# Kernel tuning notes

Measured on AMD Instinct MI355X. Metric: run time of the kernel, lower is better.

## Reference

```python
import jax, jax.numpy as jnp
import numpy as np


def setup_inputs() -> dict:
    key = jax.random.key(0)
    ks = jax.random.split(key, 5)
    N, D, H, E = 4096, 1024, 4096, 8
    x = jax.random.normal(ks[0], (N, D), dtype=jnp.float32)
    gate_w = jax.random.normal(ks[1], (D, E), dtype=jnp.float32) * (1.0 / np.sqrt(D))
    gate_b = jnp.zeros((E,), dtype=jnp.float32)
    W1 = jax.random.normal(ks[2], (E, D, H), dtype=jnp.float32) * (1.0 / np.sqrt(D))
    b1 = jnp.zeros((E, H), dtype=jnp.float32)
    W2 = jax.random.normal(ks[3], (E, H, D), dtype=jnp.float32) * (1.0 / np.sqrt(H))
    b2 = jnp.zeros((E, D), dtype=jnp.float32)
    return {"x": x, "gate_w": gate_w, "gate_b": gate_b,
            "W1": W1, "b1": b1, "W2": W2, "b2": b2}


def reference(x, gate_w, gate_b, W1, b1, W2, b2):
    # x: [N, D]; W1: [E, D, H]; W2: [E, H, D]
    K = 2
    N, D = x.shape
    E = gate_w.shape[1]
    logits = x @ gate_w + gate_b                      # [N, E]
    probs = jax.nn.softmax(logits, axis=-1)           # [N, E]
    topw, topi = jax.lax.top_k(probs, K)              # [N, K] each; raw probs, not renormalized
    # combine weights as dense [N, E] (zero for unselected experts)
    combine = jnp.zeros((N, E), dtype=x.dtype).at[jnp.arange(N)[:, None], topi].add(topw)
    # batched expert MLP over all experts (dense-dispatch; math identical to top-k combine)
    h = jnp.einsum('nd,edh->enh', x, W1) + b1[:, None, :]   # [E, N, H]
    h = jax.nn.gelu(h, approximate=True)                     # tanh-approx GELU
    y = jnp.einsum('enh,ehd->end', h, W2) + b2[:, None, :]   # [E, N, D]
    out = jnp.einsum('end,ne->nd', y, combine)               # weighted combine
    return out
```

## Files before the change

### kernel.cpp

```cpp
#include <hip/hip_runtime.h>
#include <cstdint>
#include <cstddef>

#define DEVI __device__ __forceinline__

constexpr int N_TOK = 4096, DIM = 1024, HID = 4096, NE = 8;
constexpr int NKR = N_TOK * 2;

typedef __attribute__((ext_vector_type(8))) short short8;
typedef __attribute__((ext_vector_type(4))) float f32x4;

DEVI ushort f2bf(float f) {
  union { float f; uint32_t u; } v; v.f = f;
  uint32_t r = v.u + 0x7FFFu + ((v.u >> 16) & 1u);
  return (ushort)(r >> 16);
}

DEVI float gelu_t(float x) {
  float t = 0.7978845608028654f * (x + 0.044715f * x * x * x);
  t = fminf(fmaxf(t, -15.f), 15.f);
  float e = __expf(2.f * t);
  return 0.5f * x * (1.f + (e - 1.f) / (e + 1.f));
}

DEVI void gload_lds16(const ushort* g, ushort* l) {
  __builtin_amdgcn_global_load_lds(
      (const __attribute__((address_space(1))) void*)g,
      (__attribute__((address_space(3))) void*)l, 16, 0, 0);
}

__global__ void zero_out_kernel(float* __restrict__ out, int n) {
  int i = blockIdx.x * 256 + threadIdx.x;
  if (i < n) out[i] = 0.f;
}

__global__ void convert_x_kernel(const float* __restrict__ x, ushort* __restrict__ xbf) {
  int i = (blockIdx.x * 256 + threadIdx.x) * 4;
  float4 v = *(const float4*)(x + i);
  ushort4 o;
  o.x = f2bf(v.x); o.y = f2bf(v.y); o.z = f2bf(v.z); o.w = f2bf(v.w);
  *(ushort4*)(xbf + i) = o;
}

template<int R, int C>
__global__ void transpose_bf16(const float* __restrict__ src, ushort* __restrict__ dst) {
  __shared__ ushort t[64][68];
  int e = blockIdx.z;
  const float* s = src + (size_t)e * R * C;
  ushort* d = dst + (size_t)e * R * C;
  int r0 = blockIdx.y * 64, c0 = blockIdx.x * 64;
  int lr = threadIdx.x >> 4;
  int lc = (threadIdx.x & 15) * 4;
#pragma unroll
  for (int i = 0; i < 4; ++i) {
    int r = lr + i * 16;
    float4 v = *(const float4*)(s + (size_t)(r0 + r) * C + c0 + lc);
    t[lc + 0][r] = f2bf(v.x);
    t[lc + 1][r] = f2bf(v.y);
    t[lc + 2][r] = f2bf(v.z);
    t[lc + 3][r] = f2bf(v.w);
  }
  __syncthreads();
#pragma unroll
  for (int i = 0; i < 4; ++i) {
    int c = lr + i * 16;
    ushort4 o = *(const ushort4*)&t[c][lc];
    *(ushort4*)(d + (size_t)(c0 + c) * R + r0 + lc) = o;
  }
}

__global__ void gate_kernel(const float* __restrict__ x, const float* __restrict__ gw,
                            const float* __restrict__ gb,
                            int* __restrict__ topi, float* __restrict__ topw,
                            int* __restrict__ counts) {
  int n = blockIdx.x;
  int lane = threadIdx.x;
  double p[NE];
#pragma unroll
  for (int e = 0; e < NE; ++e) p[e] = 0.0;
  const float* xr = x + (size_t)n * DIM;
  for (int d = lane; d < DIM; d += 64) {
    float xv = xr[d];
    const float* g = gw + (size_t)d * NE;
#pragma unroll
    for (int e = 0; e < NE; ++e) p[e] += (double)xv * (double)g[e];
  }
#pragma unroll
  for (int e = 0; e < NE; ++e) {
#pragma unroll
    for (int s = 32; s > 0; s >>= 1) p[e] += __shfl_down(p[e], s);
  }
  if (lane == 0) {
    double m = -1e300;
#pragma unroll
    for (int e = 0; e < NE; ++e) { p[e] += (double)gb[e]; if (p[e] > m) m = p[e]; }
    double s = 0.0, ex[NE];
#pragma unroll
    for (int e = 0; e < NE; ++e) { ex[e] = exp(p[e] - m); s += ex[e]; }
    double inv = 1.0 / s;
    int e0 = 0, e1 = 0; double v0 = -1.0, v1 = -1.0;
#pragma unroll
    for (int e = 0; e < NE; ++e) {
      double pe = ex[e] * inv;
      if (pe > v0)      { v1 = v0; e1 = e0; v0 = pe; e0 = e; }
      else if (pe > v1) { v1 = pe; e1 = e; }
    }
    topi[n * 2] = e0; topi[n * 2 + 1] = e1;
    topw[n * 2] = (float)v0; topw[n * 2 + 1] = (float)v1;
    atomicAdd(&counts[e0], 1);
    atomicAdd(&counts[e1], 1);
  }
}

__global__ void prefix_kernel(const int* __restrict__ counts, int* __restrict__ offs) {
  if (threadIdx.x == 0) {
    int s = 0;
    for (int e = 0; e < NE; ++e) { offs[e] = s; s += counts[e]; }
  }
}

__global__ void scatter_kernel(const int* __restrict__ topi, const float* __restrict__ topw,
                               const int* __restrict__ offs, int* __restrict__ fill,
                               int* __restrict__ tok, float* __restrict__ wgt) {
  int n = blockIdx.x * blockDim.x + threadIdx.x;
  if (n >= N_TOK) return;
#pragma unroll
  for (int k = 0; k < 2; ++k) {
    int e = topi[n * 2 + k];
    int pos = atomicAdd(&fill[e], 1);
    int g = offs[e] + pos;
    tok[g] = n;
    wgt[g] = topw[n * 2 + k];
  }
}

template<int K, int NX, bool FIRST>
__global__ __launch_bounds__(256) void moe_gemm(
    const ushort* __restrict__ A,
    const ushort* __restrict__ B,
    const float* __restrict__ bias,
    const int* __restrict__ tok, const float* __restrict__ wgt,
    const int* __restrict__ offs, const int* __restrict__ counts,
    ushort* __restrict__ hbuf, float* __restrict__ out)
{
  constexpr int NCOL = FIRST ? HID : DIM;
  constexpr int TSZ = 128 * 64;
  __shared__ ushort Asm[2 * TSZ];
  __shared__ ushort Bsm[2 * TSZ];

  const int nwg = NX * 32 * NE;
  const int bid = blockIdx.x;
  const int swz = (bid & 7) * (nwg >> 3) + (bid >> 3);
  const int e = swz / (NX * 32);
  const int rem = swz - e * (NX * 32);
  const int xt = rem >> 5;
  const int yt = rem & 31;

  const int cnt = counts[e];
  const int mbase = yt * 128;
  if (mbase >= cnt) return;
  const int off = offs[e];
  const int nbase = xt * 128;
  int rv = cnt - mbase; if (rv > 128) rv = 128;

  const int tid = threadIdx.x;
  const int lane = tid & 63, wave = tid >> 6;
  const int sr = tid >> 3;
  const int sc = (tid & 7) * 8;

  const ushort* arow[4];
  const ushort* brow[4];
  const ushort* Be = B + (size_t)e * ((size_t)HID * DIM) + (size_t)nbase * K;
#pragma unroll
  for (int i = 0; i < 4; ++i) {
    int r = sr + 32 * i;
    int rc = r < rv ? r : rv - 1;
    int g = off + mbase + rc;
    long t = FIRST ? (long)tok[g] : (long)g;
    arow[i] = A + t * (long)K + sc;
    brow[i] = Be + (size_t)r * K + sc;
  }

  f32x4 acc[4][4];
#pragma unroll
  for (int a = 0; a < 4; ++a)
#pragma unroll
    for (int b = 0; b < 4; ++b) acc[a][b] = (f32x4)0.f;

  const int quad = lane >> 4, lrow = lane & 15;
  const int wm = (wave >> 1) * 64, wn = (wave & 1) * 64;

  auto stage = [&](int buf, int k0) {
#pragma unroll
    for (int i = 0; i < 4; ++i) {
      gload_lds16(arow[i] + k0, &Asm[buf * TSZ + (i * 32 + wave * 8) * 64]);
      gload_lds16(brow[i] + k0, &Bsm[buf * TSZ + (i * 32 + wave * 8) * 64]);
    }
  };
  auto compute = [&](int buf) {
#pragma unroll
    for (int ks = 0; ks < 2; ++ks) {
      short8 af[4], bf[4];
#pragma unroll
      for (int mt = 0; mt < 4; ++mt)
        af[mt] = *(const short8*)&Asm[buf * TSZ + (wm + mt * 16 + lrow) * 64 + ks * 32 + quad * 8];
#pragma unroll
      for (int nt = 0; nt < 4; ++nt)
        bf[nt] = *(const short8*)&Bsm[buf * TSZ + (wn + nt * 16 + lrow) * 64 + ks * 32 + quad * 8];
#pragma unroll
      for (int mt = 0; mt < 4; ++mt)
#pragma unroll
        for (int nt = 0; nt < 4; ++nt)
          acc[mt][nt] = __builtin_amdgcn_mfma_f32_16x16x32_bf16(af[mt], bf[nt], acc[mt][nt], 0, 0, 0);
    }
  };

  constexpr int NK = K / 64;
  stage(0, 0);
  int cur = 0;
  for (int t = 0; t + 1 < NK; ++t) {
    stage(cur ^ 1, (t + 1) * 64);
    asm volatile("s_waitcnt vmcnt(8)" ::: "memory");
    __builtin_amdgcn_s_barrier();
    __builtin_amdgcn_sched_barrier(0);
    compute(cur);
    __builtin_amdgcn_sched_barrier(0);
    __builtin_amdgcn_s_barrier();
    cur ^= 1;
  }
  __syncthreads();
  compute(cur);

  if (FIRST) {
#pragma unroll
    for (int mt = 0; mt < 4; ++mt) {
#pragma unroll
      for (int i = 0; i < 4; ++i) {
        int mm = wm + mt * 16 + quad * 4 + i;
        if (mm >= rv) continue;
        size_t g = (size_t)(off + mbase + mm);
#pragma unroll
        for (int nt = 0; nt < 4; ++nt) {
          int col = nbase + wn + nt * 16 + lrow;
          float v = gelu_t(acc[mt][nt][i] + bias[e * NCOL + col]);
          hbuf[g * HID + col] = f2bf(v);
        }
      }
    }
  } else {
#pragma unroll
    for (int mt = 0; mt < 4; ++mt) {
#pragma unroll
      for (int i = 0; i < 4; ++i) {
        int mm = wm + mt * 16 + quad * 4 + i;
        if (mm >= rv) continue;
        int g = off + mbase + mm;
        long t = tok[g];
        float w = wgt[g];
#pragma unroll
        for (int nt = 0; nt < 4; ++nt) {
          int col = nbase + wn + nt * 16 + lrow;
          float v = w * (acc[mt][nt][i] + bias[e * NCOL + col]);
          atomicAdd(out + t * DIM + col, v);
        }
      }
    }
  }
}

extern "C" void kernel_launch(void* const* d_in, const int* in_sizes, int n_in,
                              void* d_out, int out_size, void* d_ws, size_t ws_size,
                              hipStream_t stream) {
  const float* x  = (const float*)d_in[0];
  const float* gw = (const float*)d_in[1];
  const float* gb = (const float*)d_in[2];
  const float* W1 = (const float*)d_in[3];
  const float* b1 = (const float*)d_in[4];
  const float* W2 = (const float*)d_in[5];
  const float* b2 = (const float*)d_in[6];
  float* out = (float*)d_out;

  char* ws = (char*)d_ws;
  size_t o = 0;
  auto alloc = [&](size_t b) { char* p = ws + o; o = (o + b + 255) & ~(size_t)255; return p; };
  int*    tok  = (int*)alloc(NKR * 4);
  float*  wgt  = (float*)alloc(NKR * 4);
  int*    topi = (int*)alloc(N_TOK * 2 * 4);
  float*  topw = (float*)alloc(N_TOK * 2 * 4);
  int*    counts = (int*)alloc(2 * NE * 4);
  int*    fill = counts + NE;
  int*    offs = (int*)alloc(NE * 4);
  ushort* xbf  = (ushort*)alloc((size_t)N_TOK * DIM * 2);
  ushort* hbuf = (ushort*)alloc((size_t)NKR * HID * 2);
  ushort* Wt   = (ushort*)alloc((size_t)NE * HID * DIM * 2);
  size_t need = o;

  zero_out_kernel<<<(out_size + 255) / 256, 256, 0, stream>>>(out, out_size);
  if (ws_size < need) return;

  hipMemsetAsync(counts, 0, 2 * NE * 4, stream);

  convert_x_kernel<<<(N_TOK * DIM / 4) / 256, 256, 0, stream>>>(x, xbf);
  gate_kernel<<<N_TOK, 64, 0, stream>>>(x, gw, gb, topi, topw, counts);
  prefix_kernel<<<1, 64, 0, stream>>>(counts, offs);
  scatter_kernel<<<(N_TOK + 255) / 256, 256, 0, stream>>>(topi, topw, offs, fill, tok, wgt);

  transpose_bf16<DIM, HID><<<dim3(HID / 64, DIM / 64, NE), 256, 0, stream>>>(W1, Wt);
  moe_gemm<DIM, HID / 128, true ><<<dim3((HID / 128) * 32 * NE), 256, 0, stream>>>(
      xbf, Wt, b1, tok, wgt, offs, counts, hbuf, out);

  transpose_bf16<HID, DIM><<<dim3(DIM / 64, HID / 64, NE), 256, 0, stream>>>(W2, Wt);
  moe_gemm<HID, DIM / 128, false><<<dim3((DIM / 128) * 32 * NE), 256, 0, stream>>>(
      hbuf, Wt, b2, tok, wgt, offs, counts, hbuf, out);
}
```

Before: 880.9 us.

## Enlarge MoE GEMM tiles to 256x256 with 8 waves and split-K for second GEMM

Grows the grouped GEMM workgroup tile from 128x128 to 256x256 using 512 threads (8 waves, each computing a 128x64 sub-tile), so more data is reused per LDS load and fewer blocks are launched. The down-projection GEMM is split along K into two parts that both accumulate into the output with atomics, with bias added only by the first split, to recover parallelism lost to the larger tiles. Block-index decoding now puts the expert in the low bits, replacing the earlier swizzle. The zeroing kernel is swapped for hipMemsetAsync. In exchange, LDS use doubles to 128 KB, register pressure rises with 32 accumulators per thread, and partially filled expert tiles waste more work.

```diff
diff --git a/kernel.cpp b/kernel.cpp
--- a/kernel.cpp
+++ b/kernel.cpp
@@ -27,11 +27,6 @@
   __builtin_amdgcn_global_load_lds(
       (const __attribute__((address_space(1))) void*)g,
       (__attribute__((address_space(3))) void*)l, 16, 0, 0);
-}
-
-__global__ void zero_out_kernel(float* __restrict__ out, int n) {
-  int i = blockIdx.x * 256 + threadIdx.x;
-  if (i < n) out[i] = 0.f;
 }
 
 __global__ void convert_x_kernel(const float* __restrict__ x, ushort* __restrict__ xbf) {
@@ -134,8 +129,8 @@
   }
 }
 
-template<int K, int NX, bool FIRST>
-__global__ __launch_bounds__(256) void moe_gemm(
+template<int K, int NXT, int KS, bool FIRST>
+__global__ __launch_bounds__(512, 2) void moe_gemm(
     const ushort* __restrict__ A,
     const ushort* __restrict__ B,
     const float* __restrict__ bias,
@@ -144,78 +139,80 @@
     ushort* __restrict__ hbuf, float* __restrict__ out)
 {
   constexpr int NCOL = FIRST ? HID : DIM;
-  constexpr int TSZ = 128 * 64;
+  constexpr int KB = K / KS;
+  constexpr int NK = KB / 64;
+  constexpr int TSZ = 256 * 64;
   __shared__ ushort Asm[2 * TSZ];
   __shared__ ushort Bsm[2 * TSZ];
 
-  const int nwg = NX * 32 * NE;
   const int bid = blockIdx.x;
-  const int swz = (bid & 7) * (nwg >> 3) + (bid >> 3);
-  const int e = swz / (NX * 32);
-  const int rem = swz - e * (NX * 32);
-  const int xt = rem >> 5;
-  const int yt = rem & 31;
+  const int e   = bid & 7;
+  const int rem = bid >> 3;
+  const int yt  = rem & 15;
+  const int xt  = (rem >> 4) % NXT;
+  const int ksp = rem / (16 * NXT);
 
   const int cnt = counts[e];
-  const int mbase = yt * 128;
+  const int mbase = yt * 256;
   if (mbase >= cnt) return;
   const int off = offs[e];
-  const int nbase = xt * 128;
-  int rv = cnt - mbase; if (rv > 128) rv = 128;
+  const int nbase = xt * 256;
+  int rv = cnt - mbase; if (rv > 256) rv = 256;
 
   const int tid = threadIdx.x;
   const int lane = tid & 63, wave = tid >> 6;
   const int sr = tid >> 3;
   const int sc = (tid & 7) * 8;
+  const int k0base = ksp * KB;
 
   const ushort* arow[4];
   const ushort* brow[4];
   const ushort* Be = B + (size_t)e * ((size_t)HID * DIM) + (size_t)nbase * K;
 #pragma unroll
   for (int i = 0; i < 4; ++i) {
-    int r = sr + 32 * i;
+    int r = sr + 64 * i;
     int rc = r < rv ? r : rv - 1;
     int g = off + mbase + rc;
     long t = FIRST ? (long)tok[g] : (long)g;
-    arow[i] = A + t * (long)K + sc;
-    brow[i] = Be + (size_t)r * K + sc;
-  }
-
-  f32x4 acc[4][4];
-#pragma unroll
-  for (int a = 0; a < 4; ++a)
+    arow[i] = A + t * (long)K + k0base + sc;
+    brow[i] = Be + (size_t)r * K + k0base + sc;
+  }
+
+  f32x4 acc[8][4];
+#pragma unroll
+  for (int a = 0; a < 8; ++a)
 #pragma unroll
     for (int b = 0; b < 4; ++b) acc[a][b] = (f32x4)0.f;
 
   const int quad = lane >> 4, lrow = lane & 15;
-  const int wm = (wave >> 1) * 64, wn = (wave & 1) * 64;
+  const int WM = (wave >> 2) * 128;
+  const int WN = (wave & 3) * 64;
 
   auto stage = [&](int buf, int k0) {
 #pragma unroll
     for (int i = 0; i < 4; ++i) {
-      gload_lds16(arow[i] + k0, &Asm[buf * TSZ + (i * 32 + wave * 8) * 64]);
-      gload_lds16(brow[i] + k0, &Bsm[buf * TSZ + (i * 32 + wave * 8) * 64]);
+      gload_lds16(arow[i] + k0, &Asm[buf * TSZ + (i * 64 + wave * 8) * 64]);
+      gload_lds16(brow[i] + k0, &Bsm[buf * TSZ + (i * 64 + wave * 8) * 64]);
     }
   };
   auto compute = [&](int buf) {
 #pragma unroll
     for (int ks = 0; ks < 2; ++ks) {
-      short8 af[4], bf[4];
-#pragma unroll
-      for (int mt = 0; mt < 4; ++mt)
-        af[mt] = *(const short8*)&Asm[buf * TSZ + (wm + mt * 16 + lrow) * 64 + ks * 32 + quad * 8];
+      short8 af[8], bf[4];
+#pragma unroll
+      for (int mt = 0; mt < 8; ++mt)
+        af[mt] = *(const short8*)&Asm[buf * TSZ + (WM + mt * 16 + lrow) * 64 + ks * 32 + quad * 8];
 #pragma unroll
       for (int nt = 0; nt < 4; ++nt)
-        bf[nt] = *(const short8*)&Bsm[buf * TSZ + (wn + nt * 16 + lrow) * 64 + ks * 32 + quad * 8];
-#pragma unroll
-      for (int mt = 0; mt < 4; ++mt)
+        bf[nt] = *(const short8*)&Bsm[buf * TSZ + (WN + nt * 16 + lrow) * 64 + ks * 32 + quad * 8];
+#pragma unroll
+      for (int mt = 0; mt < 8; ++mt)
 #pragma unroll
         for (int nt = 0; nt < 4; ++nt)
           acc[mt][nt] = __builtin_amdgcn_mfma_f32_16x16x32_bf16(af[mt], bf[nt], acc[mt][nt], 0, 0, 0);
     }
   };
 
-  constexpr int NK = K / 64;
   stage(0, 0);
   int cur = 0;
   for (int t = 0; t + 1 < NK; ++t) {
@@ -233,15 +230,15 @@
 
   if (FIRST) {
 #pragma unroll
-    for (int mt = 0; mt < 4; ++mt) {
+    for (int mt = 0; mt < 8; ++mt) {
 #pragma unroll
       for (int i = 0; i < 4; ++i) {
-        int mm = wm + mt * 16 + quad * 4 + i;
+        int mm = WM + mt * 16 + quad * 4 + i;
         if (mm >= rv) continue;
         size_t g = (size_t)(off + mbase + mm);
 #pragma unroll
         for (int nt = 0; nt < 4; ++nt) {
-          int col = nbase + wn + nt * 16 + lrow;
+          int col = nbase + WN + nt * 16 + lrow;
           float v = gelu_t(acc[mt][nt][i] + bias[e * NCOL + col]);
           hbuf[g * HID + col] = f2bf(v);
         }
@@ -249,18 +246,19 @@
     }
   } else {
 #pragma unroll
-    for (int mt = 0; mt < 4; ++mt) {
+    for (int mt = 0; mt < 8; ++mt) {
 #pragma unroll
       for (int i = 0; i < 4; ++i) {
-        int mm = wm + mt * 16 + quad * 4 + i;
+        int mm = WM + mt * 16 + quad * 4 + i;
         if (mm >= rv) continue;
         int g = off + mbase + mm;
         long t = tok[g];
         float w = wgt[g];
 #pragma unroll
         for (int nt = 0; nt < 4; ++nt) {
-          int col = nbase + wn + nt * 16 + lrow;
-          float v = w * (acc[mt][nt][i] + bias[e * NCOL + col]);
+          int col = nbase + WN + nt * 16 + lrow;
+          float bb = (ksp == 0) ? bias[e * NCOL + col] : 0.f;
+          float v = w * (acc[mt][nt][i] + bb);
           atomicAdd(out + t * DIM + col, v);
         }
       }
@@ -295,7 +293,7 @@
   ushort* Wt   = (ushort*)alloc((size_t)NE * HID * DIM * 2);
   size_t need = o;
 
-  zero_out_kernel<<<(out_size + 255) / 256, 256, 0, stream>>>(out, out_size);
+  hipMemsetAsync(out, 0, (size_t)out_size * sizeof(float), stream);
   if (ws_size < need) return;
 
   hipMemsetAsync(counts, 0, 2 * NE * 4, stream);
@@ -306,10 +304,10 @@
   scatter_kernel<<<(N_TOK + 255) / 256, 256, 0, stream>>>(topi, topw, offs, fill, tok, wgt);
 
   transpose_bf16<DIM, HID><<<dim3(HID / 64, DIM / 64, NE), 256, 0, stream>>>(W1, Wt);
-  moe_gemm<DIM, HID / 128, true ><<<dim3((HID / 128) * 32 * NE), 256, 0, stream>>>(
+  moe_gemm<DIM, HID / 256, 1, true ><<<dim3(16 * (HID / 256) * 1 * NE), 512, 0, stream>>>(
       xbf, Wt, b1, tok, wgt, offs, counts, hbuf, out);
 
   transpose_bf16<HID, DIM><<<dim3(DIM / 64, HID / 64, NE), 256, 0, stream>>>(W2, Wt);
-  moe_gemm<HID, DIM / 128, false><<<dim3((DIM / 128) * 32 * NE), 256, 0, stream>>>(
+  moe_gemm<HID, DIM / 256, 2, false><<<dim3(16 * (DIM / 256) * 2 * NE), 512, 0, stream>>>(
       hbuf, Wt, b2, tok, wgt, offs, counts, hbuf, out);
 }
```

After: 933.6 us. 6.0% more time.
